# Optimization experiments

Hardware: AMD Instinct MI355X
Metric: run time of the kernel (lower is better)

Reference implementation:

```python
import jax, jax.numpy as jnp
import numpy as np

B, N, D = 4, 4096, 1024


def setup_inputs() -> dict:
    key = jax.random.key(0)
    ks = jax.random.split(key, 7)
    s = 1.0 / np.sqrt(D)
    return {
        "x": jax.random.normal(ks[0], (B, N, D), dtype=jnp.float32),
        "Wq": jax.random.uniform(ks[1], (D, D), jnp.float32, -s, s),
        "bq": jax.random.uniform(ks[2], (D,), jnp.float32, -s, s),
        "Wk": jax.random.uniform(ks[3], (D, D), jnp.float32, -s, s),
        "bk": jax.random.uniform(ks[4], (D,), jnp.float32, -s, s),
        "Wv": jax.random.uniform(ks[5], (D, D), jnp.float32, -s, s),
        "bv": jax.random.uniform(ks[6], (D,), jnp.float32, -s, s),
    }


def reference(x, Wq, bq, Wk, bk, Wv, bv):
    # Projections (nn.Linear: x @ W.T + b; here W stored as [in, out])
    Q = x @ Wq + bq
    K = x @ Wk + bk
    V = x @ Wv + bv
    Qp = jax.nn.elu(Q) + 1.0  # positive feature map
    Kp = jax.nn.elu(K) + 1.0
    KV = jnp.einsum('bnd,bne->bde', Kp, V)          # [B, D, D]
    numerator = jnp.einsum('bnd,bde->bne', Qp, KV)  # [B, N, D]
    K_sum = Kp.sum(axis=1)                           # [B, D]
    norm = jnp.einsum('bnd,bd->bn', Qp, K_sum)[..., None]
    eps = 1e-6
    return numerator / (norm + eps)
```

## Files before the change

kernel.cpp:

```cpp
#include <hip/hip_runtime.h>
#include <hip/hip_bf16.h>
#include <cstdint>

typedef __bf16 bf16x8 __attribute__((ext_vector_type(8)));
typedef float  f32x4  __attribute__((ext_vector_type(4)));
typedef unsigned short u16x8 __attribute__((ext_vector_type(8)));

__device__ __forceinline__ unsigned short f2bf(float f) {
  __hip_bfloat16 h = __float2bfloat16(f);
  return __builtin_bit_cast(unsigned short, h);
}
__device__ __forceinline__ float bf2f(unsigned short u) {
  return __builtin_bit_cast(float, (unsigned)u << 16);
}

#define GL2LDS16(gp, lp)                                                      \
  __builtin_amdgcn_global_load_lds(                                           \
      (const __attribute__((address_space(1))) unsigned int*)(gp),            \
      (__attribute__((address_space(3))) unsigned int*)(lp), 16, 0, 0)

#define SBAR                                                                  \
  {                                                                           \
    __builtin_amdgcn_s_barrier();                                             \
    __builtin_amdgcn_sched_barrier(0);                                        \
  }
#define WAITV(n)                                                              \
  {                                                                           \
    asm volatile("s_waitcnt vmcnt(" #n ")" ::: "memory");                     \
    __builtin_amdgcn_sched_barrier(0);                                        \
  }
#define WAITL0                                                                \
  {                                                                           \
    asm volatile("s_waitcnt lgkmcnt(0)" ::: "memory");                        \
    __builtin_amdgcn_sched_barrier(0);                                        \
  }

__global__ __launch_bounds__(1024, 4) void proj_fused(
    const unsigned short* __restrict__ xb, const unsigned short* __restrict__ WT,
    unsigned short* __restrict__ QpO, unsigned short* __restrict__ KVbO,
    const float* __restrict__ bq, const float* __restrict__ bk,
    const float* __restrict__ bv) {
  __shared__ __attribute__((aligned(16))) char lds[3 * 32768];
  const int t = threadIdx.x;
  const int wave = t >> 6, lane = t & 63;
  const int wm = wave >> 2, wn = wave & 3;
  const int fr = lane & 15, fq = lane >> 4;

  const int h = blockIdx.x;
  const bool kv = (h < 512);
  const unsigned short* A;
  const unsigned short* B;
  unsigned short* Cc;
  long long ldc;
  int m0, n0;
  if (kv) {
    const int f = (h & 7) * 64 + (h >> 3);
    const int bx = f >> 3, by = f & 7;
    m0 = by * 256;
    n0 = bx * 256;
    A = WT + 1024 * 1024;
    B = xb;
    Cc = KVbO;
    ldc = 16384;
  } else {
    const int hh = h - 512;
    const int f = (hh & 7) * 32 + (hh >> 3);
    const int bx = f & 3, by = f >> 2;
    m0 = by * 256;
    n0 = bx * 256;
    A = xb;
    B = WT;
    Cc = QpO;
    ldc = 1024;
  }

  const unsigned short* gA;
  const unsigned short* gB;
  {
    int d = t * 16;
    int l = d ^ (((d >> 7) & 3) << 4);
    int row = l >> 6, kel = (l & 63) >> 1;
    gA = A + (long long)(m0 + row) * 1024 + kel;
    gB = B + (long long)(n0 + row) * 1024 + kel;
  }

  const int slotx = (fr >> 1) & 3;
  const int acore = wm * 4096 + fr * 64 + ((fq ^ slotx) << 4);
  const int bcore = 16384 + wn * 4096 + fr * 64 + ((fq ^ slotx) << 4);

  f32x4 acc[4][4];
#pragma unroll
  for (int i = 0; i < 4; ++i)
#pragma unroll
    for (int j = 0; j < 4; ++j) acc[i][j] = (f32x4){0.f, 0.f, 0.f, 0.f};

  const int NT = 32;

  auto stage = [&](int tile) {
    char* sb = lds + (tile % 3) * 32768 + wave * 1024;
    const int k0 = tile << 5;
    GL2LDS16(gA + k0, sb);
    GL2LDS16(gB + k0, sb + 16384);
  };

  stage(0);
  stage(1);
  WAITV(2);
  SBAR;

  bf16x8 av[4], bv4[4];
  for (int tt = 0; tt < NT - 2; ++tt) {
    const char* sb = lds + (tt % 3) * 32768;
    stage(tt + 2);
#pragma unroll
    for (int i = 0; i < 4; ++i) {
      av[i] = *(const bf16x8*)(sb + acore + i * 1024);
      bv4[i] = *(const bf16x8*)(sb + bcore + i * 1024);
    }
    WAITL0;
    __builtin_amdgcn_s_setprio(1);
#pragma unroll
    for (int mi = 0; mi < 4; ++mi)
#pragma unroll
      for (int ni = 0; ni < 4; ++ni)
        acc[mi][ni] = __builtin_amdgcn_mfma_f32_16x16x32_bf16(
            av[mi], bv4[ni], acc[mi][ni], 0, 0, 0);
    __builtin_amdgcn_s_setprio(0);
    WAITV(2);
    SBAR;
  }
  {
    const char* sb = lds + ((NT - 2) % 3) * 32768;
#pragma unroll
    for (int i = 0; i < 4; ++i) {
      av[i] = *(const bf16x8*)(sb + acore + i * 1024);
      bv4[i] = *(const bf16x8*)(sb + bcore + i * 1024);
    }
    WAITL0;
#pragma unroll
    for (int mi = 0; mi < 4; ++mi)
#pragma unroll
      for (int ni = 0; ni < 4; ++ni)
        acc[mi][ni] = __builtin_amdgcn_mfma_f32_16x16x32_bf16(
            av[mi], bv4[ni], acc[mi][ni], 0, 0, 0);
    WAITV(0);
    SBAR;
  }
  {
    const char* sb = lds + ((NT - 1) % 3) * 32768;
#pragma unroll
    for (int i = 0; i < 4; ++i) {
      av[i] = *(const bf16x8*)(sb + acore + i * 1024);
      bv4[i] = *(const bf16x8*)(sb + bcore + i * 1024);
    }
    WAITL0;
#pragma unroll
    for (int mi = 0; mi < 4; ++mi)
#pragma unroll
      for (int ni = 0; ni < 4; ++ni)
        acc[mi][ni] = __builtin_amdgcn_mfma_f32_16x16x32_bf16(
            av[mi], bv4[ni], acc[mi][ni], 0, 0, 0);
  }

  const bool lower = (m0 < 1024);
#pragma unroll
  for (int mi = 0; mi < 4; ++mi) {
    const int rbase = m0 + wm * 64 + mi * 16 + fq * 4;
    float rb[4];
#pragma unroll
    for (int j = 0; j < 4; ++j)
      if (kv) rb[j] = lower ? bk[rbase + j] : bv[rbase - 1024 + j];
#pragma unroll
    for (int ni = 0; ni < 4; ++ni) {
      const int c = n0 + wn * 64 + ni * 16 + fr;
      const float cb = kv ? 0.f : bq[c];
#pragma unroll
      for (int j = 0; j < 4; ++j) {
        float v = acc[mi][ni][j];
        v += kv ? rb[j] : cb;
        if (!kv || lower) v = (v > 0.f) ? v + 1.f : __expf(v);
        Cc[(long long)(rbase + j) * ldc + c] = f2bf(v);
      }
    }
  }
}

__global__ __launch_bounds__(1024, 4) void gemm_splitk(
    const unsigned short* __restrict__ A, const unsigned short* __restrict__ B,
    unsigned short* __restrict__ C) {
  __shared__ __attribute__((aligned(16))) char lds[3 * 32768];
  const int t = threadIdx.x;
  const int wave = t >> 6, lane = t & 63;
  const int wm = wave >> 2, wn = wave & 3;
  const int fr = lane & 15, fq = lane >> 4;

  const int gx = gridDim.x, gy = gridDim.y;
  int flat = blockIdx.y * gx + blockIdx.x;
  const int total = gx * gy;
  if ((total & 7) == 0) flat = (flat & 7) * (total >> 3) + (flat >> 3);
  const int bx = flat % gx, by = flat / gx;
  const int m0 = by * 256, n0 = bx * 256;

  const long long z = blockIdx.z;
  const long long koff = (z & 3) * 4096 + (z >> 2) * 1024;
  const unsigned short* Az = A + koff;
  const unsigned short* Bz = B + koff;

  const unsigned short* gA;
  const unsigned short* gB;
  {
    int d = t * 16;
    int l = d ^ (((d >> 7) & 3) << 4);
    int row = l >> 6, kel = (l & 63) >> 1;
    gA = Az + (long long)(m0 + row) * 16384 + kel;
    gB = Bz + (long long)(n0 + row) * 16384 + kel;
  }

  const int slotx = (fr >> 1) & 3;
  const int acore = wm * 4096 + fr * 64 + ((fq ^ slotx) << 4);
  const int bcore = 16384 + wn * 4096 + fr * 64 + ((fq ^ slotx) << 4);

  f32x4 acc[4][4];
#pragma unroll
  for (int i = 0; i < 4; ++i)
#pragma unroll
    for (int j = 0; j < 4; ++j) acc[i][j] = (f32x4){0.f, 0.f, 0.f, 0.f};

  const int NT = 32;

  auto stage = [&](int tile) {
    char* sb = lds + (tile % 3) * 32768 + wave * 1024;
    const int k0 = tile << 5;
    GL2LDS16(gA + k0, sb);
    GL2LDS16(gB + k0, sb + 16384);
  };

  stage(0);
  stage(1);
  WAITV(2);
  SBAR;

  bf16x8 av[4], bv[4];
  for (int tt = 0; tt < NT - 2; ++tt) {
    const char* sb = lds + (tt % 3) * 32768;
    stage(tt + 2);
#pragma unroll
    for (int i = 0; i < 4; ++i) {
      av[i] = *(const bf16x8*)(sb + acore + i * 1024);
      bv[i] = *(const bf16x8*)(sb + bcore + i * 1024);
    }
    WAITL0;
    __builtin_amdgcn_s_setprio(1);
#pragma unroll
    for (int mi = 0; mi < 4; ++mi)
#pragma unroll
      for (int ni = 0; ni < 4; ++ni)
        acc[mi][ni] = __builtin_amdgcn_mfma_f32_16x16x32_bf16(
            av[mi], bv[ni], acc[mi][ni], 0, 0, 0);
    __builtin_amdgcn_s_setprio(0);
    WAITV(2);
    SBAR;
  }
  {
    const char* sb = lds + ((NT - 2) % 3) * 32768;
#pragma unroll
    for (int i = 0; i < 4; ++i) {
      av[i] = *(const bf16x8*)(sb + acore + i * 1024);
      bv[i] = *(const bf16x8*)(sb + bcore + i * 1024);
    }
    WAITL0;
#pragma unroll
    for (int mi = 0; mi < 4; ++mi)
#pragma unroll
      for (int ni = 0; ni < 4; ++ni)
        acc[mi][ni] = __builtin_amdgcn_mfma_f32_16x16x32_bf16(
            av[mi], bv[ni], acc[mi][ni], 0, 0, 0);
    WAITV(0);
    SBAR;
  }
  {
    const char* sb = lds + ((NT - 1) % 3) * 32768;
#pragma unroll
    for (int i = 0; i < 4; ++i) {
      av[i] = *(const bf16x8*)(sb + acore + i * 1024);
      bv[i] = *(const bf16x8*)(sb + bcore + i * 1024);
    }
    WAITL0;
#pragma unroll
    for (int mi = 0; mi < 4; ++mi)
#pragma unroll
      for (int ni = 0; ni < 4; ++ni)
        acc[mi][ni] = __builtin_amdgcn_mfma_f32_16x16x32_bf16(
            av[mi], bv[ni], acc[mi][ni], 0, 0, 0);
  }

  unsigned short* Cu = C + z * 1048576ll;
#pragma unroll
  for (int mi = 0; mi < 4; ++mi) {
    const int rbase = m0 + wm * 64 + mi * 16 + fq * 4;
#pragma unroll
    for (int ni = 0; ni < 4; ++ni) {
      const int c = n0 + wn * 64 + ni * 16 + fr;
#pragma unroll
      for (int j = 0; j < 4; ++j)
        Cu[(long long)(rbase + j) * 1024 + c] = f2bf(acc[mi][ni][j]);
    }
  }
}

__global__ __launch_bounds__(512, 2) void gemm_num(
    const unsigned short* __restrict__ A, long long aOffZ,
    const unsigned short* __restrict__ B, long long bOffZ,
    float* __restrict__ C, long long cOffZ,
    const float* __restrict__ norm, long long normOffZ) {
  const long long lda = 1024, ldb = 1024, ldc = 1024;
  const int K = 1024;
  __shared__ __attribute__((aligned(16))) char lds[2 * 65536];
  const int t = threadIdx.x;
  const int wave = t >> 6, lane = t & 63;
  const int wm = wave >> 2, wn = wave & 3;
  const int fr = lane & 15, fq = lane >> 4;

  const int gx = gridDim.x, gy = gridDim.y;
  int flat = blockIdx.y * gx + blockIdx.x;
  const int total = gx * gy;
  if ((total & 7) == 0) flat = (flat & 7) * (total >> 3) + (flat >> 3);
  const int bx = flat % gx, by = flat / gx;
  const int m0 = by * 256, n0 = bx * 256;

  const long long z = blockIdx.z;
  const unsigned short* Az = A + z * aOffZ;
  const unsigned short* Bz = B + z * bOffZ;

  const unsigned short* gA[2];
  const unsigned short* gB[2];
#pragma unroll
  for (int c = 0; c < 2; ++c) {
    int d = c * 8192 + t * 16;
    int l = d ^ (((d >> 7) & 3) << 4);
    int row = l >> 6, kel = (l & 63) >> 1;
    gA[c] = Az + (long long)(m0 + row) * lda + kel;
    gB[c] = Bz + (long long)(n0 + row) * ldb + kel;
  }

  const int slotx = (fr >> 1) & 3;
  const int acore = wm * 8192 + fr * 64 + ((fq ^ slotx) << 4);
  const int bcore = wn * 4096 + fr * 64 + ((fq ^ slotx) << 4);

  f32x4 acc[8][4];
#pragma unroll
  for (int i = 0; i < 8; ++i)
#pragma unroll
    for (int j = 0; j < 4; ++j) acc[i][j] = (f32x4){0.f, 0.f, 0.f, 0.f};

  const int NT = K >> 6;

  auto stage_sub = [&](int tile, int which) {
    char* dst = lds + (tile & 1) * 65536 + which * 16384 + wave * 1024;
    const int kofs = (tile << 6) + ((which >> 1) << 5);
    if (which & 1) {
      GL2LDS16(gB[0] + kofs, dst);
      GL2LDS16(gB[1] + kofs, dst + 8192);
    } else {
      GL2LDS16(gA[0] + kofs, dst);
      GL2LDS16(gA[1] + kofs, dst + 8192);
    }
  };

  stage_sub(0, 0);
  stage_sub(0, 1);
  stage_sub(0, 2);
  stage_sub(0, 3);
  WAITV(4);
  SBAR;

  bf16x8 av[4], bv0[4], bv1[4];
  for (int tt = 0; tt < NT - 1; ++tt) {
    const char* bufp = lds + (tt & 1) * 65536;
#pragma unroll
    for (int i = 0; i < 4; ++i) {
      av[i] = *(const bf16x8*)(bufp + acore + i * 1024);
      bv0[i] = *(const bf16x8*)(bufp + 16384 + bcore + i * 1024);
    }
    stage_sub(tt + 1, 0);
    SBAR;
    WAITL0;
    __builtin_amdgcn_s_setprio(1);
#pragma unroll
    for (int mi = 0; mi < 4; ++mi)
#pragma unroll
      for (int ni = 0; ni < 4; ++ni)
        acc[mi][ni] = __builtin_amdgcn_mfma_f32_16x16x32_bf16(
            av[mi], bv0[ni], acc[mi][ni], 0, 0, 0);
    __builtin_amdgcn_s_setprio(0);
    SBAR;
#pragma unroll
    for (int i = 0; i < 4; ++i)
      av[i] = *(const bf16x8*)(bufp + acore + (4 + i) * 1024);
    stage_sub(tt + 1, 1);
    SBAR;
    WAITL0;
    __builtin_amdgcn_s_setprio(1);
#pragma unroll
    for (int mi = 0; mi < 4; ++mi)
#pragma unroll
      for (int ni = 0; ni < 4; ++ni)
        acc[4 + mi][ni] = __builtin_amdgcn_mfma_f32_16x16x32_bf16(
            av[mi], bv0[ni], acc[4 + mi][ni], 0, 0, 0);
    __builtin_amdgcn_s_setprio(0);
    WAITV(4);
    SBAR;
#pragma unroll
    for (int i = 0; i < 4; ++i) {
      av[i] = *(const bf16x8*)(bufp + 32768 + acore + i * 1024);
      bv1[i] = *(const bf16x8*)(bufp + 49152 + bcore + i * 1024);
    }
    stage_sub(tt + 1, 2);
    SBAR;
    WAITL0;
    __builtin_amdgcn_s_setprio(1);
#pragma unroll
    for (int mi = 0; mi < 4; ++mi)
#pragma unroll
      for (int ni = 0; ni < 4; ++ni)
        acc[mi][ni] = __builtin_amdgcn_mfma_f32_16x16x32_bf16(
            av[mi], bv1[ni], acc[mi][ni], 0, 0, 0);
    __builtin_amdgcn_s_setprio(0);
    SBAR;
#pragma unroll
    for (int i = 0; i < 4; ++i)
      av[i] = *(const bf16x8*)(bufp + 32768 + acore + (4 + i) * 1024);
    stage_sub(tt + 1, 3);
    SBAR;
    WAITL0;
    __builtin_amdgcn_s_setprio(1);
#pragma unroll
    for (int mi = 0; mi < 4; ++mi)
#pragma unroll
      for (int ni = 0; ni < 4; ++ni)
        acc[4 + mi][ni] = __builtin_amdgcn_mfma_f32_16x16x32_bf16(
            av[mi], bv1[ni], acc[4 + mi][ni], 0, 0, 0);
    __builtin_amdgcn_s_setprio(0);
    WAITV(4);
    SBAR;
  }
  {
    const char* bufp = lds + ((NT - 1) & 1) * 65536;
#pragma unroll
    for (int i = 0; i < 4; ++i) {
      av[i] = *(const bf16x8*)(bufp + acore + i * 1024);
      bv0[i] = *(const bf16x8*)(bufp + 16384 + bcore + i * 1024);
    }
    SBAR;
    WAITL0;
#pragma unroll
    for (int mi = 0; mi < 4; ++mi)
#pragma unroll
      for (int ni = 0; ni < 4; ++ni)
        acc[mi][ni] = __builtin_amdgcn_mfma_f32_16x16x32_bf16(
            av[mi], bv0[ni], acc[mi][ni], 0, 0, 0);
    SBAR;
#pragma unroll
    for (int i = 0; i < 4; ++i)
      av[i] = *(const bf16x8*)(bufp + acore + (4 + i) * 1024);
    SBAR;
    WAITL0;
#pragma unroll
    for (int mi = 0; mi < 4; ++mi)
#pragma unroll
      for (int ni = 0; ni < 4; ++ni)
        acc[4 + mi][ni] = __builtin_amdgcn_mfma_f32_16x16x32_bf16(
            av[mi], bv0[ni], acc[4 + mi][ni], 0, 0, 0);
    WAITV(0);
    SBAR;
#pragma unroll
    for (int i = 0; i < 4; ++i) {
      av[i] = *(const bf16x8*)(bufp + 32768 + acore + i * 1024);
      bv1[i] = *(const bf16x8*)(bufp + 49152 + bcore + i * 1024);
    }
    WAITL0;
#pragma unroll
    for (int mi = 0; mi < 4; ++mi)
#pragma unroll
      for (int ni = 0; ni < 4; ++ni)
        acc[mi][ni] = __builtin_amdgcn_mfma_f32_16x16x32_bf16(
            av[mi], bv1[ni], acc[mi][ni], 0, 0, 0);
#pragma unroll
    for (int i = 0; i < 4; ++i)
      av[i] = *(const bf16x8*)(bufp + 32768 + acore + (4 + i) * 1024);
    WAITL0;
#pragma unroll
    for (int mi = 0; mi < 4; ++mi)
#pragma unroll
      for (int ni = 0; ni < 4; ++ni)
        acc[4 + mi][ni] = __builtin_amdgcn_mfma_f32_16x16x32_bf16(
            av[mi], bv1[ni], acc[4 + mi][ni], 0, 0, 0);
  }

  const float* nrmz = norm + z * normOffZ;
  float* Cf = C + z * cOffZ;
#pragma unroll
  for (int mi = 0; mi < 8; ++mi) {
    const int rbase = m0 + wm * 128 + mi * 16 + fq * 4;
    float nv[4];
#pragma unroll
    for (int j = 0; j < 4; ++j) nv[j] = nrmz[rbase + j];
#pragma unroll
    for (int ni = 0; ni < 4; ++ni) {
      const int c = n0 + wn * 64 + ni * 16 + fr;
#pragma unroll
      for (int j = 0; j < 4; ++j)
        Cf[(long long)(rbase + j) * ldc + c] = acc[mi][ni][j] / nv[j];
    }
  }
}

__global__ __launch_bounds__(256) void prep_fused(
    const float* __restrict__ Wq, const float* __restrict__ Wk,
    const float* __restrict__ Wv, unsigned short* __restrict__ WT,
    const float4* __restrict__ x4, uint2* __restrict__ xb4) {
  __shared__ float tile[32][33];
  if (blockIdx.z < 3) {
    const float* W = blockIdx.z == 0 ? Wq : (blockIdx.z == 1 ? Wk : Wv);
    unsigned short* out = WT + (size_t)blockIdx.z * 1024 * 1024;
    const int tx = threadIdx.x & 31, ty = threadIdx.x >> 5;
    const int i0 = blockIdx.y * 32, o0 = blockIdx.x * 32;
#pragma unroll
    for (int s = 0; s < 32; s += 8)
      tile[ty + s][tx] = W[(long long)(i0 + ty + s) * 1024 + o0 + tx];
    __syncthreads();
#pragma unroll
    for (int s = 0; s < 32; s += 8)
      out[(long long)(o0 + ty + s) * 1024 + i0 + tx] = f2bf(tile[tx][ty + s]);
  } else {
    const int flat = blockIdx.y * 32 + blockIdx.x;
    const int n4 = 4194304;
    for (int i = flat * 256 + threadIdx.x; i < n4; i += 1024 * 256) {
      float4 v = x4[i];
      uint2 o;
      o.x = (unsigned)f2bf(v.x) | ((unsigned)f2bf(v.y) << 16);
      o.y = (unsigned)f2bf(v.z) | ((unsigned)f2bf(v.w) << 16);
      xb4[i] = o;
    }
  }
}

__global__ __launch_bounds__(256) void ksum_kernel(
    const unsigned short* __restrict__ KpT, float* __restrict__ Ksum) {
  const int gw = (blockIdx.x * 256 + threadIdx.x) >> 6;
  const int lane = threadIdx.x & 63;
  const int d = gw >> 2, b = gw & 3;
  const unsigned short* p = KpT + (long long)d * 16384 + b * 4096 + lane * 8;
  float s = 0.f;
#pragma unroll
  for (int it = 0; it < 8; ++it) {
    u16x8 v = *(const u16x8*)(p + it * 512);
#pragma unroll
    for (int j = 0; j < 8; ++j) s += bf2f(v[j]);
  }
#pragma unroll
  for (int o = 32; o > 0; o >>= 1) s += __shfl_down(s, o, 64);
  if (lane == 0) Ksum[b * 1024 + d] = s;
}

__global__ __launch_bounds__(256) void tail_fused(
    const unsigned short* __restrict__ P, unsigned short* __restrict__ KVt,
    const unsigned short* __restrict__ Qp, const float* __restrict__ Ksum,
    float* __restrict__ nrm) {
  if (blockIdx.x < 2048) {
    const long long i = ((long long)blockIdx.x * 256 + threadIdx.x) * 8;
    const int b = (int)(i >> 20);
    const long long ed = i & ((1ll << 20) - 1);
    float s[8] = {0.f, 0.f, 0.f, 0.f, 0.f, 0.f, 0.f, 0.f};
#pragma unroll
    for (int ks = 0; ks < 4; ++ks) {
      u16x8 v = *(const u16x8*)(P + ((long long)(ks * 4 + b) << 20) + ed);
#pragma unroll
      for (int j = 0; j < 8; ++j) s[j] += bf2f(v[j]);
    }
    u16x8 o;
#pragma unroll
    for (int j = 0; j < 8; ++j) o[j] = f2bf(s[j]);
    *(u16x8*)(KVt + i) = o;
  } else {
    const int gw = ((blockIdx.x - 2048) * 256 + threadIdx.x) >> 6;
    const int lane = threadIdx.x & 63;
    const int b = gw >> 12;
    const unsigned short* q = Qp + (long long)gw * 1024 + lane * 8;
    const float* ks = Ksum + b * 1024 + lane * 8;
    float s = 0.f;
#pragma unroll
    for (int it = 0; it < 2; ++it) {
      u16x8 v = *(const u16x8*)(q + it * 512);
      float4 k0 = *(const float4*)(ks + it * 512);
      float4 k1 = *(const float4*)(ks + it * 512 + 4);
      s += bf2f(v[0]) * k0.x + bf2f(v[1]) * k0.y + bf2f(v[2]) * k0.z +
           bf2f(v[3]) * k0.w + bf2f(v[4]) * k1.x + bf2f(v[5]) * k1.y +
           bf2f(v[6]) * k1.z + bf2f(v[7]) * k1.w;
    }
#pragma unroll
    for (int o = 32; o > 0; o >>= 1) s += __shfl_down(s, o, 64);
    if (lane == 0) nrm[gw] = s + 1e-6f;
  }
}

extern "C" void kernel_launch(void* const* d_in, const int* in_sizes, int n_in,
                              void* d_out, int out_size, void* d_ws,
                              size_t ws_size, hipStream_t stream) {
  const float* x  = (const float*)d_in[0];
  const float* Wq = (const float*)d_in[1];
  const float* bq = (const float*)d_in[2];
  const float* Wk = (const float*)d_in[3];
  const float* bk = (const float*)d_in[4];
  const float* Wv = (const float*)d_in[5];
  const float* bv = (const float*)d_in[6];
  float* out = (float*)d_out;

  const size_t MN = 16384ull * 1024ull;
  char* w = (char*)d_ws;
  unsigned short* xb  = (unsigned short*)w;  w += MN * 2;
  unsigned short* WT  = (unsigned short*)w;  w += 3ull * 1024 * 1024 * 2;
  unsigned short* Qp  = (unsigned short*)w;  w += MN * 2;
  unsigned short* KVb = (unsigned short*)w;  w += 2 * MN * 2;
  unsigned short* KVt = (unsigned short*)w;  w += 4ull * 1024 * 1024 * 2;
  float* Ksum = (float*)w;  w += 4ull * 1024 * 4;
  float* nrm  = (float*)w;  w += 16384ull * 4;
  unsigned short* Pkv = xb;
  unsigned short* KpT = KVb;
  unsigned short* VT  = KVb + MN;

  prep_fused<<<dim3(32, 32, 4), 256, 0, stream>>>(Wq, Wk, Wv, WT,
                                                  (const float4*)x, (uint2*)xb);
  proj_fused<<<768, 1024, 0, stream>>>(xb, WT, Qp, KVb, bq, bk, bv);
  ksum_kernel<<<1024, 256, 0, stream>>>(KpT, Ksum);
  gemm_splitk<<<dim3(4, 4, 16), 1024, 0, stream>>>(VT, KpT, Pkv);
  tail_fused<<<6144, 256, 0, stream>>>(Pkv, KVt, Qp, Ksum, nrm);
  gemm_num<<<dim3(4, 16, 4), 512, 0, stream>>>(
      Qp, 4096ll * 1024, KVt, 1024 * 1024, out, 4096ll * 1024, nrm, 4096);
}
```

Measured before the change: 238.5 us.

## Fold Ksum into split-K GEMM and compute norm inside numerator GEMM

Removes the standalone ksum kernel by adding an extra z-slice of blocks to the split-K KV GEMM that computes the column sums of Kp. The per-row normalizer Qp·Ksum is now computed at the start of gemm_num into shared memory, so tail_fused shrinks to a pure split-K reduction. This cuts one kernel launch and the global round-trip of the norm buffer, at the cost of each gemm_num block re-reading its 256 Qp rows before the main loop. The Ksum blocks share the launch shape of the GEMM, including its 1024-thread blocks and LDS allocation.

```diff
diff --git a/kernel.cpp b/kernel.cpp
--- a/kernel.cpp
+++ b/kernel.cpp
@@ -185,12 +185,34 @@
   }
 }
 
-__global__ __launch_bounds__(1024, 4) void gemm_splitk(
+__global__ __launch_bounds__(1024, 4) void splitk_ksum(
     const unsigned short* __restrict__ A, const unsigned short* __restrict__ B,
-    unsigned short* __restrict__ C) {
+    unsigned short* __restrict__ C, float* __restrict__ Ksum) {
   __shared__ __attribute__((aligned(16))) char lds[3 * 32768];
   const int t = threadIdx.x;
   const int wave = t >> 6, lane = t & 63;
+
+  if (blockIdx.z == 16) {
+    const int wtask = (blockIdx.y * 4 + blockIdx.x) * 16 + wave;
+#pragma unroll
+    for (int rr = 0; rr < 16; ++rr) {
+      const int gw = wtask * 16 + rr;
+      const int d = gw >> 2, b = gw & 3;
+      const unsigned short* p = B + (long long)d * 16384 + b * 4096 + lane * 8;
+      float s = 0.f;
+#pragma unroll
+      for (int it = 0; it < 8; ++it) {
+        u16x8 v = *(const u16x8*)(p + it * 512);
+#pragma unroll
+        for (int j = 0; j < 8; ++j) s += bf2f(v[j]);
+      }
+#pragma unroll
+      for (int o = 32; o > 0; o >>= 1) s += __shfl_down(s, o, 64);
+      if (lane == 0) Ksum[b * 1024 + d] = s;
+    }
+    return;
+  }
+
   const int wm = wave >> 2, wn = wave & 3;
   const int fr = lane & 15, fq = lane >> 4;
 
@@ -294,7 +316,7 @@
             av[mi], bv[ni], acc[mi][ni], 0, 0, 0);
   }
 
-  unsigned short* Cu = C + z * 1048576ll;
+  unsigned short* Cu = C + blockIdx.z * 1048576ll;
 #pragma unroll
   for (int mi = 0; mi < 4; ++mi) {
     const int rbase = m0 + wm * 64 + mi * 16 + fq * 4;
@@ -312,10 +334,11 @@
     const unsigned short* __restrict__ A, long long aOffZ,
     const unsigned short* __restrict__ B, long long bOffZ,
     float* __restrict__ C, long long cOffZ,
-    const float* __restrict__ norm, long long normOffZ) {
+    const float* __restrict__ Ksum) {
   const long long lda = 1024, ldb = 1024, ldc = 1024;
   const int K = 1024;
   __shared__ __attribute__((aligned(16))) char lds[2 * 65536];
+  __shared__ float snrm[256];
   const int t = threadIdx.x;
   const int wave = t >> 6, lane = t & 63;
   const int wm = wave >> 2, wn = wave & 3;
@@ -331,6 +354,29 @@
   const long long z = blockIdx.z;
   const unsigned short* Az = A + z * aOffZ;
   const unsigned short* Bz = B + z * bOffZ;
+
+  {
+    const float* ks = Ksum + z * 1024 + lane * 8;
+    const float4 k0a = *(const float4*)(ks);
+    const float4 k1a = *(const float4*)(ks + 4);
+    const float4 k0b = *(const float4*)(ks + 512);
+    const float4 k1b = *(const float4*)(ks + 516);
+    for (int r = wave; r < 256; r += 8) {
+      const unsigned short* q = Az + (long long)(m0 + r) * 1024 + lane * 8;
+      u16x8 v0 = *(const u16x8*)(q);
+      u16x8 v1 = *(const u16x8*)(q + 512);
+      float s = bf2f(v0[0]) * k0a.x + bf2f(v0[1]) * k0a.y +
+                bf2f(v0[2]) * k0a.z + bf2f(v0[3]) * k0a.w +
+                bf2f(v0[4]) * k1a.x + bf2f(v0[5]) * k1a.y +
+                bf2f(v0[6]) * k1a.z + bf2f(v0[7]) * k1a.w;
+      s += bf2f(v1[0]) * k0b.x + bf2f(v1[1]) * k0b.y + bf2f(v1[2]) * k0b.z +
+           bf2f(v1[3]) * k0b.w + bf2f(v1[4]) * k1b.x + bf2f(v1[5]) * k1b.y +
+           bf2f(v1[6]) * k1b.z + bf2f(v1[7]) * k1b.w;
+#pragma unroll
+      for (int o = 32; o > 0; o >>= 1) s += __shfl_down(s, o, 64);
+      if (lane == 0) snrm[r] = s + 1e-6f;
+    }
+  }
 
   const unsigned short* gA[2];
   const unsigned short* gB[2];
@@ -497,14 +543,14 @@
             av[mi], bv1[ni], acc[4 + mi][ni], 0, 0, 0);
   }
 
-  const float* nrmz = norm + z * normOffZ;
   float* Cf = C + z * cOffZ;
 #pragma unroll
   for (int mi = 0; mi < 8; ++mi) {
     const int rbase = m0 + wm * 128 + mi * 16 + fq * 4;
+    const int rloc = wm * 128 + mi * 16 + fq * 4;
     float nv[4];
 #pragma unroll
-    for (int j = 0; j < 4; ++j) nv[j] = nrmz[rbase + j];
+    for (int j = 0; j < 4; ++j) nv[j] = snrm[rloc + j];
 #pragma unroll
     for (int ni = 0; ni < 4; ++ni) {
       const int c = n0 + wn * 64 + ni * 16 + fr;
@@ -545,63 +591,22 @@
   }
 }
 
-__global__ __launch_bounds__(256) void ksum_kernel(
-    const unsigned short* __restrict__ KpT, float* __restrict__ Ksum) {
-  const int gw = (blockIdx.x * 256 + threadIdx.x) >> 6;
-  const int lane = threadIdx.x & 63;
-  const int d = gw >> 2, b = gw & 3;
-  const unsigned short* p = KpT + (long long)d * 16384 + b * 4096 + lane * 8;
-  float s = 0.f;
-#pragma unroll
-  for (int it = 0; it < 8; ++it) {
-    u16x8 v = *(const u16x8*)(p + it * 512);
-#pragma unroll
-    for (int j = 0; j < 8; ++j) s += bf2f(v[j]);
-  }
-#pragma unroll
-  for (int o = 32; o > 0; o >>= 1) s += __shfl_down(s, o, 64);
-  if (lane == 0) Ksum[b * 1024 + d] = s;
-}
-
-__global__ __launch_bounds__(256) void tail_fused(
-    const unsigned short* __restrict__ P, unsigned short* __restrict__ KVt,
-    const unsigned short* __restrict__ Qp, const float* __restrict__ Ksum,
-    float* __restrict__ nrm) {
-  if (blockIdx.x < 2048) {
-    const long long i = ((long long)blockIdx.x * 256 + threadIdx.x) * 8;
-    const int b = (int)(i >> 20);
-    const long long ed = i & ((1ll << 20) - 1);
-    float s[8] = {0.f, 0.f, 0.f, 0.f, 0.f, 0.f, 0.f, 0.f};
-#pragma unroll
-    for (int ks = 0; ks < 4; ++ks) {
-      u16x8 v = *(const u16x8*)(P + ((long long)(ks * 4 + b) << 20) + ed);
-#pragma unroll
-      for (int j = 0; j < 8; ++j) s[j] += bf2f(v[j]);
-    }
-    u16x8 o;
-#pragma unroll
-    for (int j = 0; j < 8; ++j) o[j] = f2bf(s[j]);
-    *(u16x8*)(KVt + i) = o;
-  } else {
-    const int gw = ((blockIdx.x - 2048) * 256 + threadIdx.x) >> 6;
-    const int lane = threadIdx.x & 63;
-    const int b = gw >> 12;
-    const unsigned short* q = Qp + (long long)gw * 1024 + lane * 8;
-    const float* ks = Ksum + b * 1024 + lane * 8;
-    float s = 0.f;
-#pragma unroll
-    for (int it = 0; it < 2; ++it) {
-      u16x8 v = *(const u16x8*)(q + it * 512);
-      float4 k0 = *(const float4*)(ks + it * 512);
-      float4 k1 = *(const float4*)(ks + it * 512 + 4);
-      s += bf2f(v[0]) * k0.x + bf2f(v[1]) * k0.y + bf2f(v[2]) * k0.z +
-           bf2f(v[3]) * k0.w + bf2f(v[4]) * k1.x + bf2f(v[5]) * k1.y +
-           bf2f(v[6]) * k1.z + bf2f(v[7]) * k1.w;
-    }
-#pragma unroll
-    for (int o = 32; o > 0; o >>= 1) s += __shfl_down(s, o, 64);
-    if (lane == 0) nrm[gw] = s + 1e-6f;
-  }
+__global__ __launch_bounds__(256) void reduce_kvt(
+    const unsigned short* __restrict__ P, unsigned short* __restrict__ KVt) {
+  const long long i = ((long long)blockIdx.x * 256 + threadIdx.x) * 8;
+  const int b = (int)(i >> 20);
+  const long long ed = i & ((1ll << 20) - 1);
+  float s[8] = {0.f, 0.f, 0.f, 0.f, 0.f, 0.f, 0.f, 0.f};
+#pragma unroll
+  for (int ks = 0; ks < 4; ++ks) {
+    u16x8 v = *(const u16x8*)(P + ((long long)(ks * 4 + b) << 20) + ed);
+#pragma unroll
+    for (int j = 0; j < 8; ++j) s[j] += bf2f(v[j]);
+  }
+  u16x8 o;
+#pragma unroll
+  for (int j = 0; j < 8; ++j) o[j] = f2bf(s[j]);
+  *(u16x8*)(KVt + i) = o;
 }
 
 extern "C" void kernel_launch(void* const* d_in, const int* in_sizes, int n_in,
@@ -624,7 +629,6 @@
   unsigned short* KVb = (unsigned short*)w;  w += 2 * MN * 2;
   unsigned short* KVt = (unsigned short*)w;  w += 4ull * 1024 * 1024 * 2;
   float* Ksum = (float*)w;  w += 4ull * 1024 * 4;
-  float* nrm  = (float*)w;  w += 16384ull * 4;
   unsigned short* Pkv = xb;
   unsigned short* KpT = KVb;
   unsigned short* VT  = KVb + MN;
@@ -632,9 +636,8 @@
   prep_fused<<<dim3(32, 32, 4), 256, 0, stream>>>(Wq, Wk, Wv, WT,
                                                   (const float4*)x, (uint2*)xb);
   proj_fused<<<768, 1024, 0, stream>>>(xb, WT, Qp, KVb, bq, bk, bv);
-  ksum_kernel<<<1024, 256, 0, stream>>>(KpT, Ksum);
-  gemm_splitk<<<dim3(4, 4, 16), 1024, 0, stream>>>(VT, KpT, Pkv);
-  tail_fused<<<6144, 256, 0, stream>>>(Pkv, KVt, Qp, Ksum, nrm);
+  splitk_ksum<<<dim3(4, 4, 17), 1024, 0, stream>>>(VT, KpT, Pkv, Ksum);
+  reduce_kvt<<<2048, 256, 0, stream>>>(Pkv, KVt);
   gemm_num<<<dim3(4, 16, 4), 512, 0, stream>>>(
-      Qp, 4096ll * 1024, KVt, 1024 * 1024, out, 4096ll * 1024, nrm, 4096);
-}
+      Qp, 4096ll * 1024, KVt, 1024 * 1024, out, 4096ll * 1024, Ksum);
+}
```

Result: slower. 263.9 us (+10.6%).
